# Kernel tuning notes

Measured on AMD Instinct MI355X. Metric: run time of the kernel, lower is better.

Reference implementation:

```python
import jax, jax.numpy as jnp
import numpy as np

D_MODEL = 2048
N_HEADS = 16
D_K = D_MODEL // N_HEADS
BATCH = 4
SEQ = 2048


def setup_inputs() -> dict:
    key = jax.random.key(0)
    ks = jax.random.split(key, 9)
    s = 1.0 / np.sqrt(D_MODEL)
    return {
        "x": jax.random.normal(ks[0], (BATCH, SEQ, D_MODEL), dtype=jnp.float32),
        "wq_w": jax.random.normal(ks[1], (D_MODEL, D_MODEL), dtype=jnp.float32) * s,
        "wq_b": jax.random.normal(ks[2], (D_MODEL,), dtype=jnp.float32) * 0.02,
        "wk_w": jax.random.normal(ks[3], (D_MODEL, D_MODEL), dtype=jnp.float32) * s,
        "wk_b": jax.random.normal(ks[4], (D_MODEL,), dtype=jnp.float32) * 0.02,
        "wv_w": jax.random.normal(ks[5], (D_MODEL, D_MODEL), dtype=jnp.float32) * s,
        "wv_b": jax.random.normal(ks[6], (D_MODEL,), dtype=jnp.float32) * 0.02,
        "wo_w": jax.random.normal(ks[7], (D_MODEL, D_MODEL), dtype=jnp.float32) * s,
        "wo_b": jax.random.normal(ks[8], (D_MODEL,), dtype=jnp.float32) * 0.02,
    }


def reference(x, wq_w, wq_b, wk_w, wk_b, wv_w, wv_b, wo_w, wo_b):
    b, s, _ = x.shape
    # Linear projections (torch Linear: x @ W^T + b)
    def split_heads(t):  # (b, s, d_model) -> (b, h, s, d_k)
        return t.reshape(b, s, N_HEADS, D_K).transpose(0, 2, 1, 3)
    q = split_heads(x @ wq_w.T + wq_b)
    k = split_heads(x @ wk_w.T + wk_b)
    v = split_heads(x @ wv_w.T + wv_b)
    scale = 1.0 / jnp.sqrt(jnp.asarray(D_K, dtype=x.dtype))
    scores = jnp.einsum("bhqd,bhkd->bhqk", q, k) * scale  # (b, h, s, s)
    attn = jax.nn.softmax(scores, axis=-1)
    ctx = jnp.einsum("bhqk,bhkd->bhqd", attn, v)
    ctx = ctx.transpose(0, 2, 1, 3).reshape(b, s, D_MODEL)
    out = ctx @ wo_w.T + wo_b
    return out
```

## Files before the change

### kernel.cpp

```cpp
#include <hip/hip_runtime.h>
#include <hip/hip_bf16.h>
#include <math.h>

typedef __attribute__((ext_vector_type(8))) short short8;
typedef __attribute__((ext_vector_type(4))) float f32x4;
typedef __attribute__((ext_vector_type(16))) float f32x16;
typedef __attribute__((ext_vector_type(4))) unsigned short u16x4;
typedef __attribute__((ext_vector_type(8))) unsigned short u16x8;
typedef __attribute__((ext_vector_type(4))) unsigned int u32x4;
typedef __attribute__((ext_vector_type(2))) int i32x2;
typedef unsigned short u16;
typedef unsigned int u32;

#define DM 2048
#define SQ 2048
#define NB 4
#define NH 16
#define DKH 128
#define KT 64
#define NT (SQ / KT)
#define LD2 (2 * DM)
#define NROW (NB * SQ)
#define QSCALE (0.08838834764831845f * 1.4426950408889634f)

__device__ __forceinline__ u16 f2bf(float f) {
  unsigned u = __float_as_uint(f);
  u += 0x7fffu + ((u >> 16) & 1u);
  return (u16)(u >> 16);
}

__device__ __forceinline__ u32 cvtpk(float lo, float hi) {
  u32 r;
  asm("v_cvt_pk_bf16_f32 %0, %1, %2" : "=v"(r) : "v"(lo), "v"(hi));
  return r;
}

__device__ __forceinline__ void gload16(const u16* g, u16* lds) {
  __builtin_amdgcn_global_load_lds(
      (const __attribute__((address_space(1))) unsigned int*)g,
      (__attribute__((address_space(3))) unsigned int*)lds, 16, 0, 0);
}

__device__ __forceinline__ int paddr16(int r, int k, int nkt) {
  const int cid = (((r >> 8) * nkt + (k >> 6)) << 5) | (((r >> 7) & 1) << 4) |
                  (((r >> 5) & 3) << 2) | ((k >> 4) & 3);
  return (cid << 9) + (((r & 31) | (((k >> 3) & 1) << 3 << 2)) << 3) + (k & 7);
}

__device__ __forceinline__ void pinv(int idx, int nkt, int& r, int& k) {
  const int e8 = idx & 63;
  const int cid = idx >> 6;
  const int kt = (cid >> 5) % nkt;
  const int rt = (cid >> 5) / nkt;
  r = (rt << 8) + (((cid >> 4) & 1) << 7) + (((cid >> 2) & 3) << 5) + (e8 & 31);
  k = (kt << 6) + ((cid & 3) << 4) + ((e8 >> 5) << 3);
}

__global__ void cvt_x_p(const float* __restrict__ in, u16* __restrict__ out) {
  const int idx = blockIdx.x * 256 + threadIdx.x;
  int r, k;
  pinv(idx, 32, r, k);
  const float4 v0 = *(const float4*)(in + (size_t)r * DM + k);
  const float4 v1 = *(const float4*)(in + (size_t)r * DM + k + 4);
  u16x8 o;
  o[0] = f2bf(v0.x); o[1] = f2bf(v0.y); o[2] = f2bf(v0.z); o[3] = f2bf(v0.w);
  o[4] = f2bf(v1.x); o[5] = f2bf(v1.y); o[6] = f2bf(v1.z); o[7] = f2bf(v1.w);
  *(u16x8*)(out + (size_t)idx * 8) = o;
}

__global__ void cvt_w_p(const float* __restrict__ w0, const float* __restrict__ w1,
                        const float* __restrict__ w2, const float* __restrict__ w3,
                        u16* __restrict__ dq, u16* __restrict__ dw) {
  const int sel = blockIdx.y;
  const float* src;
  switch (sel) {
    case 0: src = w0; break;
    case 1: src = w1; break;
    case 2: src = w2; break;
    default: src = w3; break;
  }
  const int idx = blockIdx.x * 256 + threadIdx.x;
  int r, k;
  pinv(idx, 32, r, k);
  const float4 v0 = *(const float4*)(src + (size_t)r * DM + k);
  const float4 v1 = *(const float4*)(src + (size_t)r * DM + k + 4);
  u16x8 o;
  o[0] = f2bf(v0.x); o[1] = f2bf(v0.y); o[2] = f2bf(v0.z); o[3] = f2bf(v0.w);
  o[4] = f2bf(v1.x); o[5] = f2bf(v1.y); o[6] = f2bf(v1.z); o[7] = f2bf(v1.w);
  u16* dst = (sel < 3) ? (dq + (size_t)sel * DM * DM) : dw;
  *(u16x8*)(dst + (size_t)idx * 8) = o;
}


#define STG_A(T, HALF)                                                       \
  do {                                                                       \
    _Pragma("unroll") for (int uu = 0; uu < 2; ++uu) {                       \
      const int j_ = w * 2 + uu;                                             \
      gload16(As + ((((T) * 32 + (HALF) * 16 + j_) << 9) + l * 8),           \
              &smA[((T) & 1) * 16384 + ((HALF) * 16 + j_) * 512]);           \
    }                                                                        \
  } while (0)

#define STG_B(T, HALF)                                                       \
  do {                                                                       \
    _Pragma("unroll") for (int uu = 0; uu < 2; ++uu) {                       \
      const int j_ = w * 2 + uu;                                             \
      gload16(Bs + ((((T) * 32 + (HALF) * 16 + j_) << 9) + l * 8),           \
              &smB[((T) & 1) * 16384 + ((HALF) * 16 + j_) * 512]);           \
    }                                                                        \
  } while (0)

#define LDA(QM)                                                            \
  do {                                                                     \
    const int rb_ = wr * 4 + (QM) * 2;                                     \
    const u16* p_ = &smA[bi * 16384 + rb_ * 2048 + l * 8];                 \
    _Pragma("unroll") for (int s = 0; s < 4; ++s) {                        \
      af[0][s] = *(const short8*)&p_[s * 512];                             \
      af[1][s] = *(const short8*)&p_[2048 + s * 512];                      \
    }                                                                      \
  } while (0)

#define LDB(QN)                                                            \
  do {                                                                     \
    const int rb_ = wc * 2 + (QN);                                         \
    const u16* p_ = &smB[bi * 16384 + rb_ * 2048 + l * 8];                 \
    _Pragma("unroll") for (int s = 0; s < 4; ++s)                          \
      bf[QN][s] = *(const short8*)&p_[s * 512];                            \
  } while (0)

#define MFMA_Q(QM, QN)                                                             \
  __builtin_amdgcn_s_setprio(1);                                                   \
  _Pragma("unroll") for (int s = 0; s < 4; ++s) {                                  \
    acc[(QM) * 2][(QN)] = __builtin_amdgcn_mfma_f32_32x32x16_bf16(                 \
        af[0][s], bf[QN][s], acc[(QM) * 2][(QN)], 0, 0, 0);                        \
    acc[(QM) * 2 + 1][(QN)] = __builtin_amdgcn_mfma_f32_32x32x16_bf16(             \
        af[1][s], bf[QN][s], acc[(QM) * 2 + 1][(QN)], 0, 0, 0);                    \
  }                                                                                \
  __builtin_amdgcn_s_setprio(0);

template <int MODE>
__global__ __launch_bounds__(512, 2) void gemm8p(
    const u16* __restrict__ A, const u16* __restrict__ B,
    const float* __restrict__ bq, const float* __restrict__ bk,
    const float* __restrict__ bvp, void* __restrict__ Cout,
    void* __restrict__ Cout2, int M, int N, int K) {
  __shared__ u16 smA[2 * 16384];
  __shared__ u16 smB[2 * 16384];
  const int tid = threadIdx.x;
  const int w = tid >> 6, l = tid & 63;
  const int c5 = l & 31, hi = l >> 5;
  const int wr = w >> 2, wc = w & 3;

  int flat = blockIdx.x + (int)gridDim.x * (int)blockIdx.y;
  const int nwg = (int)(gridDim.x * gridDim.y);
  flat = (flat & 7) * (nwg >> 3) + (flat >> 3);
  const int m0 = (flat / (int)gridDim.x) * 256, n0 = (flat % (int)gridDim.x) * 256;

  const int NSTEP = K / 64;
  f32x16 acc[4][2] = {};

  const u16* As = A + (size_t)(m0 >> 8) * NSTEP * 16384;
  const u16* Bs = B + (size_t)(n0 >> 8) * NSTEP * 16384;

  STG_A(0, 0); STG_A(0, 1); STG_B(0, 0); STG_B(0, 1);
  STG_B(1, 0); STG_A(1, 0);
  asm volatile("s_waitcnt vmcnt(4)" ::: "memory");
  __builtin_amdgcn_s_barrier();

  short8 af[2][4], bf[2][4];
  for (int t = 0; t < NSTEP; ++t) {
    const int bi = t & 1;
    LDA(0); LDB(0);
    if (t + 1 < NSTEP) STG_B(t + 1, 1);
    MFMA_Q(0, 0);
    __builtin_amdgcn_s_barrier();
    LDB(1);
    if (t + 1 < NSTEP) STG_A(t + 1, 1);
    MFMA_Q(0, 1);
    __builtin_amdgcn_s_barrier();
    LDA(1);
    if (t + 2 < NSTEP) STG_B(t + 2, 0);
    MFMA_Q(1, 1);
    __builtin_amdgcn_s_barrier();
    if (t + 2 < NSTEP) STG_A(t + 2, 0);
    MFMA_Q(1, 0);
    if (t + 2 < NSTEP)
      asm volatile("s_waitcnt vmcnt(4)" ::: "memory");
    else if (t + 1 < NSTEP)
      asm volatile("s_waitcnt vmcnt(0)" ::: "memory");
    __builtin_amdgcn_s_barrier();
  }

#pragma unroll
  for (int nf = 0; nf < 2; ++nf) {
    const int col = n0 + wc * 64 + nf * 32 + c5;
    if (MODE == 0) {
      const int seg = col >> 11;
      const float* bp = seg == 0 ? bq : (seg == 1 ? bk : bvp);
      const float bval = bp[col & (DM - 1)];
      const float os = (seg == 0) ? QSCALE : 1.0f;
      if (seg < 2) {
#pragma unroll
        for (int mf = 0; mf < 4; ++mf)
#pragma unroll
          for (int r = 0; r < 16; ++r) {
            const int row = m0 + wr * 128 + mf * 32 + (r & 3) + 8 * (r >> 2) + 4 * hi;
            ((u16*)Cout)[(size_t)row * LD2 + col] = f2bf((acc[mf][nf][r] + bval) * os);
          }
      } else {
        u16* vbase = (u16*)Cout2 + (size_t)(col - 2 * DM) * NROW;
#pragma unroll
        for (int mf = 0; mf < 4; ++mf) {
          const int row0 = m0 + wr * 128 + mf * 32 + 4 * hi;
#pragma unroll
          for (int g2 = 0; g2 < 4; ++g2) {
            u16x4 pk;
#pragma unroll
            for (int j = 0; j < 4; ++j)
              pk[j] = f2bf(acc[mf][nf][g2 * 4 + j] + bval);
            *(u16x4*)(vbase + row0 + 8 * g2) = pk;
          }
        }
      }
    } else {
      const float bval = bq[col];
#pragma unroll
      for (int mf = 0; mf < 4; ++mf)
#pragma unroll
        for (int r = 0; r < 16; ++r) {
          const int row = m0 + wr * 128 + mf * 32 + (r & 3) + 8 * (r >> 2) + 4 * hi;
          ((float*)Cout)[(size_t)row * N + col] = acc[mf][nf][r] + bval;
        }
    }
  }
}

__global__ __launch_bounds__(512, 2) void attn(
    const u16* __restrict__ QK, const u16* __restrict__ VT, u16* __restrict__ O) {
  __shared__ u16 smK[2 * 8192];
  __shared__ u16 smV[2 * 8192];
  __shared__ float alScr[8 * 32];

  const u16* Qp = QK;
  const u16* Kp = QK + DM;

  const int tid = threadIdx.x;
  const int w = tid >> 6, l = tid & 63;
  const int c5 = l & 31, hi = l >> 5;

  int flat = blockIdx.x + ((int)blockIdx.y << 3) + ((int)blockIdx.z << 7);
  flat = (flat & 7) * 64 + (flat >> 3);
  const int qt = flat & 7, h = (flat >> 3) & 15, b = flat >> 7;

  const int q0 = qt * 256 + w * 32;
  const size_t rowb = (size_t)b * SQ;
  const int hoff = h * DKH;

  short8 qf[8];
#pragma unroll
  for (int ds = 0; ds < 8; ++ds)
    qf[ds] = *(const short8*)&Qp[(rowb + q0 + c5) * LD2 + hoff + ds * 16 + hi * 8];

  f32x16 o[4] = {};
  float mrow = -1e30f, lsum = 0.f;

  const u16* vsrc = VT + (size_t)(hoff + (l >> 3)) * NROW + rowb + ((l & 7) ^ (l >> 3)) * 8;

  {
#pragma unroll
    for (int uu = 0; uu < 2; ++uu) {
      const int u = w * 2 + uu;
      const int row = u * 4 + (l >> 4);
      const int col16 = (l & 15) ^ (row & 15);
      gload16(&Kp[(rowb + row) * LD2 + hoff + col16 * 8], &smK[u * 512]);
      gload16(vsrc + (size_t)u * 8 * NROW, &smV[u * 512]);
    }
  }
  __syncthreads();

  int buf = 0;
  for (int t = 0; t < NT; ++t) {
    const int nb = buf ^ 1;
    if (t + 1 < NT) {
      const size_t kvr = rowb + (size_t)(t + 1) * KT;
      const int kv1 = (t + 1) * KT;
#pragma unroll
      for (int uu = 0; uu < 2; ++uu) {
        const int u = w * 2 + uu;
        const int row = u * 4 + (l >> 4);
        const int col16 = (l & 15) ^ (row & 15);
        gload16(&Kp[(kvr + row) * LD2 + hoff + col16 * 8], &smK[nb * 8192 + u * 512]);
        gload16(vsrc + (size_t)u * 8 * NROW + kv1, &smV[nb * 8192 + u * 512]);
      }
    }

    f32x16 s[2] = {};
    __builtin_amdgcn_s_setprio(1);
#pragma unroll
    for (int ds = 0; ds < 8; ++ds) {
#pragma unroll
      for (int ni = 0; ni < 2; ++ni) {
        const int row = ni * 32 + c5;
        const short8 kf = *(const short8*)&smK[buf * 8192 + row * 128 + (((ds << 1) | hi) ^ (row & 15)) * 8];
        s[ni] = __builtin_amdgcn_mfma_f32_32x32x16_bf16(kf, qf[ds], s[ni], 0, 0, 0);
      }
    }
    __builtin_amdgcn_s_setprio(0);

    float mt[16];
#pragma unroll
    for (int i = 0; i < 16; ++i) mt[i] = fmaxf(s[0][i], s[1][i]);
#pragma unroll
    for (int st = 8; st >= 1; st >>= 1)
#pragma unroll
      for (int i = 0; i < st; ++i) mt[i] = fmaxf(mt[i], mt[i + st]);
    i32x2 sw = __builtin_amdgcn_permlane32_swap(__float_as_int(mt[0]), __float_as_int(mt[0]), false, false);
    const float gmax = fmaxf(__int_as_float(sw.x), __int_as_float(sw.y));

    if (__any(gmax > mrow + 10.0f)) {
      const float mn = fmaxf(mrow, gmax);
      const float al = exp2f(mrow - mn);
      mrow = mn;
      lsum *= al;
      alScr[w * 32 + c5] = al;
#pragma unroll
      for (int r = 0; r < 16; ++r) {
        const float av = alScr[w * 32 + (r & 3) + 8 * (r >> 2) + 4 * hi];
#pragma unroll
        for (int dg = 0; dg < 4; ++dg) o[dg][r] *= av;
      }
    }

    float ps0 = 0.f, ps1 = 0.f;
#pragma unroll
    for (int i = 0; i < 16; ++i) {
      const float p0 = exp2f(s[0][i] - mrow);
      const float p1 = exp2f(s[1][i] - mrow);
      s[0][i] = p0; s[1][i] = p1;
      ps0 += p0; ps1 += p1;
    }
    lsum += ps0 + ps1;

    __builtin_amdgcn_s_setprio(1);
#pragma unroll
    for (int ks = 0; ks < 4; ++ks) {
      const int b0_ = (ks & 1) * 8;
      const int ni = ks >> 1;
      const u32 A0 = cvtpk(s[ni][b0_ + 0], s[ni][b0_ + 1]);
      const u32 A1 = cvtpk(s[ni][b0_ + 4], s[ni][b0_ + 5]);
      const u32 B0 = cvtpk(s[ni][b0_ + 2], s[ni][b0_ + 3]);
      const u32 B1 = cvtpk(s[ni][b0_ + 6], s[ni][b0_ + 7]);
      const i32x2 r0 = __builtin_amdgcn_permlane32_swap((int)A0, (int)A1, false, false);
      const i32x2 r1 = __builtin_amdgcn_permlane32_swap((int)B0, (int)B1, false, false);
      u32x4 paw;
      paw.x = (u32)r0.x; paw.y = (u32)r1.x; paw.z = (u32)r0.y; paw.w = (u32)r1.y;
      const short8 pa = *(const short8*)&paw;
#pragma unroll
      for (int dg = 0; dg < 4; ++dg) {
        const int rowd = dg * 32 + c5;
        const short8 vf = *(const short8*)&smV[buf * 8192 + rowd * 64 + (((ks * 2 + hi) ^ (c5 & 7))) * 8];
        o[dg] = __builtin_amdgcn_mfma_f32_32x32x16_bf16(pa, vf, o[dg], 0, 0, 0);
      }
    }
    __builtin_amdgcn_s_setprio(0);

    __syncthreads();
    buf = nb;
  }

  {
    const i32x2 sl = __builtin_amdgcn_permlane32_swap(__float_as_int(lsum), __float_as_int(lsum), false, false);
    const float tot = __int_as_float(sl.x) + __int_as_float(sl.y);
    alScr[w * 32 + c5] = 1.0f / tot;
  }
#pragma unroll
  for (int r = 0; r < 16; ++r) {
    const int qloc = (r & 3) + 8 * (r >> 2) + 4 * hi;
    const float inv = alScr[w * 32 + qloc];
    const int rowg = (int)rowb + q0 + qloc;
#pragma unroll
    for (int dg = 0; dg < 4; ++dg)
      O[paddr16(rowg, hoff + dg * 32 + c5, 32)] = f2bf(o[dg][r] * inv);
  }
}

extern "C" void kernel_launch(void* const* d_in, const int* in_sizes, int n_in,
                              void* d_out, int out_size, void* d_ws, size_t ws_size,
                              hipStream_t stream) {
  const float* x    = (const float*)d_in[0];
  const float* wq_w = (const float*)d_in[1];
  const float* wq_b = (const float*)d_in[2];
  const float* wk_w = (const float*)d_in[3];
  const float* wk_b = (const float*)d_in[4];
  const float* wv_w = (const float*)d_in[5];
  const float* wv_b = (const float*)d_in[6];
  const float* wo_w = (const float*)d_in[7];
  const float* wo_b = (const float*)d_in[8];
  float* out = (float*)d_out;

  u16* p = (u16*)d_ws;
  u16* xb  = p; p += (size_t)NROW * DM;
  u16* wqb = p; p += (size_t)3 * DM * DM;
  u16* wob = p; p += (size_t)DM * DM;
  u16* QKb = p; p += (size_t)NROW * LD2;
  u16* VTb = p; p += (size_t)DM * NROW;
  u16* ctx = xb;

  cvt_x_p<<<dim3(NROW * DM / 2048), dim3(256), 0, stream>>>(x, xb);
  cvt_w_p<<<dim3(DM * DM / 2048, 4), dim3(256), 0, stream>>>(wq_w, wk_w, wv_w, wo_w, wqb, wob);

  dim3 gg3(3 * DM / 256, NROW / 256);
  gemm8p<0><<<gg3, dim3(512), 0, stream>>>(xb, wqb, wq_b, wk_b, wv_b, QKb, VTb,
                                           NROW, 3 * DM, DM);

  attn<<<dim3(SQ / 256, NH, NB), dim3(512), 0, stream>>>(QKb, VTb, ctx);

  dim3 ggo(DM / 256, NROW / 256);
  gemm8p<1><<<ggo, dim3(512), 0, stream>>>(ctx, wob, wo_b, nullptr, nullptr, out,
                                           nullptr, NROW, DM, DM);
}
```

Baseline: 549.6 us.

## Restructure attention into 128-query blocks with split K/V pipelining, fuse conversion kernels

The attention kernel now runs 256-thread blocks covering 128 queries each, so twice as many blocks are launched. V moves to a single LDS buffer loaded after each iteration's PV step, while K stays double-buffered. Explicit vmcnt waits and raw barriers replace __syncthreads so the QK^T and softmax work can overlap with the in-flight V load. The two fp32-to-bf16 conversion kernels are merged into one launch to save launch overhead. The risks are that hand-counted vmcnt values could race if the compiler reorders loads, and that smaller blocks reload K/V more often per query.

```diff
diff --git a/kernel.cpp b/kernel.cpp
--- a/kernel.cpp
+++ b/kernel.cpp
@@ -21,6 +21,8 @@
 #define NT (SQ / KT)
 #define LD2 (2 * DM)
 #define NROW (NB * SQ)
+#define NX8 (NROW * DM / 8)
+#define NW8 (DM * DM / 8)
 #define QSCALE (0.08838834764831845f * 1.4426950408889634f)
 
 __device__ __forceinline__ u16 f2bf(float f) {
@@ -56,30 +58,24 @@
   k = (kt << 6) + ((cid & 3) << 4) + ((e8 >> 5) << 3);
 }
 
-__global__ void cvt_x_p(const float* __restrict__ in, u16* __restrict__ out) {
-  const int idx = blockIdx.x * 256 + threadIdx.x;
-  int r, k;
-  pinv(idx, 32, r, k);
-  const float4 v0 = *(const float4*)(in + (size_t)r * DM + k);
-  const float4 v1 = *(const float4*)(in + (size_t)r * DM + k + 4);
-  u16x8 o;
-  o[0] = f2bf(v0.x); o[1] = f2bf(v0.y); o[2] = f2bf(v0.z); o[3] = f2bf(v0.w);
-  o[4] = f2bf(v1.x); o[5] = f2bf(v1.y); o[6] = f2bf(v1.z); o[7] = f2bf(v1.w);
-  *(u16x8*)(out + (size_t)idx * 8) = o;
-}
-
-__global__ void cvt_w_p(const float* __restrict__ w0, const float* __restrict__ w1,
+__global__ void cvt_all(const float* __restrict__ x,
+                        const float* __restrict__ w0, const float* __restrict__ w1,
                         const float* __restrict__ w2, const float* __restrict__ w3,
-                        u16* __restrict__ dq, u16* __restrict__ dw) {
-  const int sel = blockIdx.y;
+                        u16* __restrict__ xb, u16* __restrict__ wqb,
+                        u16* __restrict__ wob) {
+  const int gid = blockIdx.x * 256 + threadIdx.x;
   const float* src;
-  switch (sel) {
-    case 0: src = w0; break;
-    case 1: src = w1; break;
-    case 2: src = w2; break;
-    default: src = w3; break;
-  }
-  const int idx = blockIdx.x * 256 + threadIdx.x;
+  u16* dst;
+  int idx;
+  if (gid < NX8) {
+    src = x; dst = xb; idx = gid;
+  } else {
+    const int t = gid - NX8;
+    const int sel = t / NW8;
+    idx = t - sel * NW8;
+    src = sel == 0 ? w0 : sel == 1 ? w1 : sel == 2 ? w2 : w3;
+    dst = (sel < 3) ? (wqb + (size_t)sel * DM * DM) : wob;
+  }
   int r, k;
   pinv(idx, 32, r, k);
   const float4 v0 = *(const float4*)(src + (size_t)r * DM + k);
@@ -87,7 +83,6 @@
   u16x8 o;
   o[0] = f2bf(v0.x); o[1] = f2bf(v0.y); o[2] = f2bf(v0.z); o[3] = f2bf(v0.w);
   o[4] = f2bf(v1.x); o[5] = f2bf(v1.y); o[6] = f2bf(v1.z); o[7] = f2bf(v1.w);
-  u16* dst = (sel < 3) ? (dq + (size_t)sel * DM * DM) : dw;
   *(u16x8*)(dst + (size_t)idx * 8) = o;
 }
 
@@ -235,11 +230,11 @@
   }
 }
 
-__global__ __launch_bounds__(512, 2) void attn(
+__global__ __launch_bounds__(256) void attn(
     const u16* __restrict__ QK, const u16* __restrict__ VT, u16* __restrict__ O) {
   __shared__ u16 smK[2 * 8192];
-  __shared__ u16 smV[2 * 8192];
-  __shared__ float alScr[8 * 32];
+  __shared__ u16 smV[8192];
+  __shared__ float alScr[4 * 32];
 
   const u16* Qp = QK;
   const u16* Kp = QK + DM;
@@ -248,11 +243,11 @@
   const int w = tid >> 6, l = tid & 63;
   const int c5 = l & 31, hi = l >> 5;
 
-  int flat = blockIdx.x + ((int)blockIdx.y << 3) + ((int)blockIdx.z << 7);
-  flat = (flat & 7) * 64 + (flat >> 3);
-  const int qt = flat & 7, h = (flat >> 3) & 15, b = flat >> 7;
-
-  const int q0 = qt * 256 + w * 32;
+  int flat = blockIdx.x + ((int)blockIdx.y << 4) + ((int)blockIdx.z << 8);
+  flat = (flat & 7) * 128 + (flat >> 3);
+  const int qt = flat & 15, h = (flat >> 4) & 15, b = flat >> 8;
+
+  const int q0 = qt * 128 + w * 32;
   const size_t rowb = (size_t)b * SQ;
   const int hoff = h * DKH;
 
@@ -268,31 +263,38 @@
 
   {
 #pragma unroll
-    for (int uu = 0; uu < 2; ++uu) {
-      const int u = w * 2 + uu;
+    for (int uu = 0; uu < 4; ++uu) {
+      const int u = w * 4 + uu;
       const int row = u * 4 + (l >> 4);
       const int col16 = (l & 15) ^ (row & 15);
       gload16(&Kp[(rowb + row) * LD2 + hoff + col16 * 8], &smK[u * 512]);
+    }
+#pragma unroll
+    for (int uu = 0; uu < 4; ++uu) {
+      const int u = w * 4 + uu;
       gload16(vsrc + (size_t)u * 8 * NROW, &smV[u * 512]);
     }
   }
-  __syncthreads();
+  asm volatile("s_waitcnt vmcnt(0)" ::: "memory");
+  __builtin_amdgcn_s_barrier();
 
   int buf = 0;
   for (int t = 0; t < NT; ++t) {
     const int nb = buf ^ 1;
     if (t + 1 < NT) {
       const size_t kvr = rowb + (size_t)(t + 1) * KT;
-      const int kv1 = (t + 1) * KT;
-#pragma unroll
-      for (int uu = 0; uu < 2; ++uu) {
-        const int u = w * 2 + uu;
+#pragma unroll
+      for (int uu = 0; uu < 4; ++uu) {
+        const int u = w * 4 + uu;
         const int row = u * 4 + (l >> 4);
         const int col16 = (l & 15) ^ (row & 15);
         gload16(&Kp[(kvr + row) * LD2 + hoff + col16 * 8], &smK[nb * 8192 + u * 512]);
-        gload16(vsrc + (size_t)u * 8 * NROW + kv1, &smV[nb * 8192 + u * 512]);
-      }
-    }
+      }
+      asm volatile("s_waitcnt vmcnt(8)" ::: "memory");
+    } else {
+      asm volatile("s_waitcnt vmcnt(4)" ::: "memory");
+    }
+    __builtin_amdgcn_sched_barrier(0);
 
     f32x16 s[2] = {};
     __builtin_amdgcn_s_setprio(1);
@@ -340,6 +342,13 @@
       ps0 += p0; ps1 += p1;
     }
     lsum += ps0 + ps1;
+
+    if (t + 1 < NT)
+      asm volatile("s_waitcnt vmcnt(4)" ::: "memory");
+    else
+      asm volatile("s_waitcnt vmcnt(0)" ::: "memory");
+    __builtin_amdgcn_s_barrier();
+    __builtin_amdgcn_sched_barrier(0);
 
     __builtin_amdgcn_s_setprio(1);
 #pragma unroll
@@ -358,13 +367,21 @@
 #pragma unroll
       for (int dg = 0; dg < 4; ++dg) {
         const int rowd = dg * 32 + c5;
-        const short8 vf = *(const short8*)&smV[buf * 8192 + rowd * 64 + (((ks * 2 + hi) ^ (c5 & 7))) * 8];
+        const short8 vf = *(const short8*)&smV[rowd * 64 + (((ks * 2 + hi) ^ (rowd & 7))) * 8];
         o[dg] = __builtin_amdgcn_mfma_f32_32x32x16_bf16(pa, vf, o[dg], 0, 0, 0);
       }
     }
     __builtin_amdgcn_s_setprio(0);
 
-    __syncthreads();
+    __builtin_amdgcn_s_barrier();
+    if (t + 1 < NT) {
+      const int kv1 = (t + 1) * KT;
+#pragma unroll
+      for (int uu = 0; uu < 4; ++uu) {
+        const int u = w * 4 + uu;
+        gload16(vsrc + (size_t)u * 8 * NROW + kv1, &smV[u * 512]);
+      }
+    }
     buf = nb;
   }
 
@@ -406,14 +423,14 @@
   u16* VTb = p; p += (size_t)DM * NROW;
   u16* ctx = xb;
 
-  cvt_x_p<<<dim3(NROW * DM / 2048), dim3(256), 0, stream>>>(x, xb);
-  cvt_w_p<<<dim3(DM * DM / 2048, 4), dim3(256), 0, stream>>>(wq_w, wk_w, wv_w, wo_w, wqb, wob);
+  cvt_all<<<dim3((NX8 + 4 * NW8) / 256), dim3(256), 0, stream>>>(
+      x, wq_w, wk_w, wv_w, wo_w, xb, wqb, wob);
 
   dim3 gg3(3 * DM / 256, NROW / 256);
   gemm8p<0><<<gg3, dim3(512), 0, stream>>>(xb, wqb, wq_b, wk_b, wv_b, QKb, VTb,
                                            NROW, 3 * DM, DM);
 
-  attn<<<dim3(SQ / 256, NH, NB), dim3(512), 0, stream>>>(QKb, VTb, ctx);
+  attn<<<dim3(SQ / 128, NH, NB), dim3(256), 0, stream>>>(QKb, VTb, ctx);
 
   dim3 ggo(DM / 256, NROW / 256);
   gemm8p<1><<<ggo, dim3(512), 0, stream>>>(ctx, wob, wo_b, nullptr, nullptr, out,
```

After: 623.3 us. 1.13x slower.
